# Kernel tuning notes

Measured on AMD Instinct MI355X. Metric: run time of the kernel, lower is better.

The kernel has to match this reference:

```python
import jax, jax.numpy as jnp
import numpy as np

MESH_SIZE = 0.01
HIDDEN = 256
NUM_LAYERS = 3
TEMP = 1e-3          # soft-relay temperature (forward default)
H_SCALE = 0.0        # soft-magnet: mu0*H << B
M_SCALE = 0.5
M_OFFSET = 0.5


def _make_mesh():
    # Uniform triangular Preisach mesh: points (beta, alpha) with 0 <= beta <= alpha <= 1.
    k = int(round(1.0 / MESH_SIZE)) + 1  # 101 grid lines -> 5151 points
    g = np.linspace(0.0, 1.0, k, dtype=np.float32)
    bb, aa = np.meshgrid(g, g, indexing='ij')
    sel = bb <= aa
    return jnp.asarray(np.stack([bb[sel], aa[sel]], axis=-1))  # [N, 2] = (beta, alpha)


def setup_inputs() -> dict:
    key = jax.random.key(0)
    ks = jax.random.split(key, 10)
    mesh = _make_mesh()                       # [N, 2]
    n = mesh.shape[0]
    B, CTXT, T = 8, 128, 2048
    encoder_input = jax.random.uniform(ks[0], (B, CTXT, 2), dtype=jnp.float32)
    decoder_input = jax.random.uniform(ks[1], (B, T, 1), dtype=jnp.float32)
    initial_states = 2.0 * jax.random.uniform(ks[2], (B, n), dtype=jnp.float32) - 1.0  # s in [-1, 1]
    y0 = jax.random.uniform(ks[3], (B,), dtype=jnp.float32)
    # ResNetMLP density network params (input_dim=2, output_dim=1)
    W_in = jax.random.normal(ks[4], (2, HIDDEN), dtype=jnp.float32) * 0.5
    b_in = jnp.zeros((HIDDEN,), dtype=jnp.float32)
    W_blk = jax.random.normal(ks[5], (NUM_LAYERS, HIDDEN, HIDDEN), dtype=jnp.float32) * (1.0 / np.sqrt(HIDDEN))
    b_blk = jnp.zeros((NUM_LAYERS, HIDDEN), dtype=jnp.float32)
    W_out = jax.random.normal(ks[6], (HIDDEN, 1), dtype=jnp.float32) * (1.0 / np.sqrt(HIDDEN))
    b_out = jnp.zeros((1,), dtype=jnp.float32)
    return {'encoder_input': encoder_input, 'decoder_input': decoder_input,
            'initial_states': initial_states, 'y0': y0, 'mesh': mesh,
            'W_in': W_in, 'b_in': b_in, 'W_blk': W_blk, 'b_blk': b_blk,
            'W_out': W_out, 'b_out': b_out}


def _density(mesh, W_in, b_in, W_blk, b_blk, W_out, b_out):
    # ResNetMLP (eval: dropout off) + sigmoid (normalized_density=True)
    h = jax.nn.relu(mesh @ W_in + b_in)
    for i in range(NUM_LAYERS):  # small fixed layer loop
        h = h + jax.nn.relu(h @ W_blk[i] + b_blk[i])
    return jax.nn.sigmoid((h @ W_out + b_out)[..., 0])  # [N]


def _get_states(h_seq, alpha, beta, s0, h0):
    # Sequential soft-relay hysteron update across time.
    # h_seq [B,T], alpha/beta [N], s0 [B,N], h0 [B]
    def step(carry, h_t):  # h_t [B]
        s, h_prev = carry
        up = jax.nn.sigmoid((h_t[:, None] - alpha[None, :]) / TEMP)   # switch to +1 when h > alpha
        dn = jax.nn.sigmoid((h_t[:, None] - beta[None, :]) / TEMP)    # stay/unswitch vs beta when sweeping down
        s_up = s + (1.0 - s) * up            # increasing field branch
        s_dn = -1.0 + (s + 1.0) * dn         # decreasing field branch
        inc = (h_t >= h_prev)[:, None]
        s_new = jnp.where(inc, s_up, s_dn)
        return (s_new, h_t), s_new
    (_, _), states = jax.lax.scan(step, (s0, h0), jnp.swapaxes(h_seq, 0, 1))
    return jnp.swapaxes(states, 0, 1)  # [B, T, N]


def reference(encoder_input, decoder_input, initial_states, y0, mesh,
              W_in, b_in, W_blk, b_blk, W_out, b_out):
    B = encoder_input.shape[0]
    n = mesh.shape[0]
    beta = mesh[:, 0]
    alpha = mesh[:, 1]
    density = _density(mesh, W_in, b_in, W_blk, b_blk, W_out, b_out)  # [N] (shared mesh, eval)
    h = decoder_input[..., 0]                                          # [B, T]
    states = _get_states(h, alpha, beta, initial_states, y0)           # [B, T, N]
    m = jnp.einsum('n,btn->bt', density, states) / jnp.sum(density)    # [B, T]
    b_norm = H_SCALE * h + M_SCALE * m + M_OFFSET
    density_b = jnp.broadcast_to(density, (B, n))
    mesh_b = jnp.broadcast_to(mesh, (B,) + mesh.shape)
    return (b_norm, density_b, m, initial_states, mesh_b)
```

## Files before the change

kernel.cpp:

```cpp
#include <hip/hip_runtime.h>
#include <hip/hip_fp16.h>
#include <math.h>

#define N_MESH   5151
#define NB       8
#define TT       2048
#define HID      256
#define NLAYERS  3
#define NCHUNK   64
#define CHUNK    32
#define NQ       11
#define NPAD     5632
#define SCAN_GRID 512
#define PREP_NBLK 48
#define COPY_NBLK 61
#define MLP_NBLK  81
#define PH2_NBLK  88
#define DENSB_NBLK 21

#define OFF_TP    144
#define SMEM1     656
#define OFF_RED   656
#define OFF_DRED  5264
#define SMEM3     5392

#define WS_DENSITY 0
#define WS_WT      6144
#define WS_PQ      104448

#define OUT_BNORM  0
#define OUT_DENSB  16384
#define OUT_M      57592
#define OUT_S0     73976
#define OUT_MESHB  115184

typedef _Float16 half8  __attribute__((ext_vector_type(8)));
typedef float    f32x4  __attribute__((ext_vector_type(4)));

__device__ __forceinline__ float sigmoid_fast(float x) {
    float e = __expf(-x);
    return __builtin_amdgcn_rcpf(1.0f + e);
}

__device__ __forceinline__ int swz(int row, int kbyte) {
    return row * 512 + (kbyte ^ ((row & 7) << 4));
}

__device__ __forceinline__ float dpp16_sum(float v) {
    int a;
    a = __builtin_amdgcn_update_dpp(0, __float_as_int(v), 0xB1, 0xF, 0xF, true);
    v += __int_as_float(a);
    a = __builtin_amdgcn_update_dpp(0, __float_as_int(v), 0x4E, 0xF, 0xF, true);
    v += __int_as_float(a);
    a = __builtin_amdgcn_update_dpp(0, __float_as_int(v), 0x141, 0xF, 0xF, true);
    v += __int_as_float(a);
    a = __builtin_amdgcn_update_dpp(0, __float_as_int(v), 0x140, 0xF, 0xF, true);
    v += __int_as_float(a);
    return v;
}

__device__ __forceinline__ void build_params(int tid, const float* hs2,
                                             float4* tp)
{
    if (tid < CHUNK) {
        float ht = hs2[tid + 1];
        float hp = hs2[tid];
        bool inc = (ht >= hp);
        float sg = inc ? 1.f : -1.f;
        float psg = sg;
        if (tid > 0) psg = (hs2[tid] >= hs2[tid - 1]) ? 1.f : -1.f;
        float x = ht * 1000.f;
        float gc = rintf(ht * 100.f);
        float4 p;
        p.x = psg - sg;
        if (inc) {
            float Ac = sigmoid_fast(fmaf(10.f, gc, -x));
            p.y = 1.f;  p.z = Ac - gc;
        } else {
            float Ac = sigmoid_fast(fmaf(-10.f, gc, x));
            p.y = -1.f; p.z = gc + Ac;
        }
        p.w = sg;
        tp[tid] = p;
    }
}

__global__ __launch_bounds__(512, 4) void k1_scan1_prep(
    const float* __restrict__ dec, const float* __restrict__ y0,
    const float* __restrict__ mesh, const float* __restrict__ Wblk,
    float2* __restrict__ PQ, half8* __restrict__ WT,
    const float* __restrict__ s0, float* __restrict__ out)
{
    __shared__ __align__(16) char smem[SMEM1];
    const int tid = threadIdx.x;
    const int bid = blockIdx.x;

    if (bid >= SCAN_GRID + PREP_NBLK) {
        int idx = bid - (SCAN_GRID + PREP_NBLK);
        const int n1 = NB * N_MESH;
        const int total = 3 * n1;
#pragma unroll
        for (int k = 0; k < 4; ++k) {
            int j = idx * 2048 + k * 512 + tid;
            if (j < total) {
                if (j < n1) out[OUT_S0 + j] = s0[j];
                else {
                    int jj = j - n1;
                    out[OUT_MESHB + jj] = mesh[jj % (2 * N_MESH)];
                }
            }
        }
        return;
    }

    if (bid >= SCAN_GRID) {
        int g = (bid - SCAN_GRID) * 512 + tid;
        int l  = g & 63;
        int nt = (g >> 6) & 15;
        int kg = (g >> 10) & 7;
        int L  = g >> 13;
        int n  = nt * 16 + (l & 15);
        int kb = kg * 32 + ((l >> 4) & 3) * 8;
        const float* Wb = Wblk + (size_t)L * HID * HID;
        half8 v;
#pragma unroll
        for (int i = 0; i < 8; ++i)
            v[i] = (_Float16)Wb[(size_t)(kb + i) * HID + n];
        WT[g] = v;
        return;
    }

    float* hs2 = (float*)smem;
    float4* tp = (float4*)(smem + OFF_TP);

    const int b = bid & 7;
    const int c = bid >> 3;
    const int t0 = c * CHUNK;

    if (tid < CHUNK) hs2[tid + 1] = dec[b * TT + t0 + tid];
    if (tid == 0) hs2[0] = (c == 0) ? y0[b] : dec[b * TT + t0 - 1];

    float fga[NQ], fgb[NQ];
#pragma unroll
    for (int q = 0; q < NQ; ++q) {
        int n = q * 512 + tid;
        if (n < N_MESH) {
            fgb[q] = rintf(mesh[2 * n]     * 100.0f);
            fga[q] = rintf(mesh[2 * n + 1] * 100.0f);
        } else { fga[q] = 0.f; fgb[q] = 0.f; }
    }
    __syncthreads();
    build_params(tid, hs2, tp);
    __syncthreads();

    float P[NQ], R[NQ];
    float sg0 = tp[0].w;
#pragma unroll
    for (int q = 0; q < NQ; ++q) { P[q] = 1.f; R[q] = -sg0; }

    for (int tb = 0; tb < CHUNK; tb += 8) {
#pragma unroll
        for (int j = 0; j < 8; ++j) {
            float4 p = tp[tb + j];
            bool inc = p.y > 0.f;
#pragma unroll
            for (int q = 0; q < NQ; ++q) {
                float gq = inc ? fga[q] : fgb[q];
                float A = __builtin_amdgcn_fmed3f(fmaf(p.y, gq, p.z), 0.f, 1.f);
                float r = R[q] + p.x;
                P[q] *= A;
                R[q] = r * A;
            }
        }
    }
    float sgl = tp[CHUNK - 1].w;
    size_t basew = ((size_t)(c * NB + b)) * NPAD;
#pragma unroll
    for (int q = 0; q < NQ; ++q) {
        float2 v; v.x = P[q]; v.y = R[q] + sgl;
        PQ[basew + q * 512 + tid] = v;
    }
}

__global__ __launch_bounds__(512) void k2_mlp_phase2(
    const float* __restrict__ mesh, const float* __restrict__ Win,
    const float* __restrict__ bin,  const half8* __restrict__ WT,
    const float* __restrict__ bblk, const float* __restrict__ Wout,
    const float* __restrict__ bout, float* __restrict__ density,
    const float* __restrict__ s0_in, float* __restrict__ PQf)
{
    __shared__ __align__(16) char hA[64 * 512];
    __shared__ float psum[4][16][2];
    const int tid  = threadIdx.x;

    if (blockIdx.x >= MLP_NBLK) {
        int idx = blockIdx.x - MLP_NBLK;
        int nbb = idx % NQ;
        int b   = idx / NQ;
        int n   = nbb * 512 + tid;
        const float2* PQ = (const float2*)PQf;
        float s = (n < N_MESH) ? s0_in[b * N_MESH + n] : 0.f;
#pragma unroll 4
        for (int c = 0; c < NCHUNK; ++c) {
            size_t ix = ((size_t)(c * NB + b)) * NPAD + n;
            float2 pv = PQ[ix];
            PQf[2 * ix] = s;
            s = fmaf(pv.x, s, pv.y);
        }
        return;
    }

    const int w    = tid >> 6;
    const int lane = tid & 63;
    const int rl   = lane & 15;
    const int cg   = lane >> 4;
    const int mt   = w & 3;
    const int nh   = w >> 2;
    const int row0 = blockIdx.x * 64;

    float hreg[8][4];

    {
        float m0[4], m1[4];
#pragma unroll
        for (int r = 0; r < 4; ++r) {
            int gr = row0 + mt * 16 + cg * 4 + r;
            if (gr < N_MESH) { m0[r] = mesh[2 * gr]; m1[r] = mesh[2 * gr + 1]; }
            else { m0[r] = 0.f; m1[r] = 0.f; }
        }
#pragma unroll
        for (int j = 0; j < 8; ++j) {
            int col = nh * 128 + j * 16 + rl;
            float wa = Win[col], wb = Win[HID + col], bi = bin[col];
#pragma unroll
            for (int r = 0; r < 4; ++r) {
                float v = fmaxf(fmaf(m0[r], wa, fmaf(m1[r], wb, bi)), 0.f);
                hreg[j][r] = v;
                *(_Float16*)(hA + swz(mt * 16 + cg * 4 + r, col * 2)) =
                    (_Float16)v;
            }
        }
    }
    __syncthreads();

    for (int L = 0; L < NLAYERS; ++L) {
        half8 af[8];
#pragma unroll
        for (int kg = 0; kg < 8; ++kg)
            af[kg] = *(const half8*)(hA + swz(mt * 16 + rl, kg * 64 + cg * 16));
        __syncthreads();

        float bias[8];
#pragma unroll
        for (int j = 0; j < 8; ++j)
            bias[j] = bblk[L * HID + nh * 128 + j * 16 + rl];

        f32x4 acc[8];
#pragma unroll
        for (int j = 0; j < 8; ++j) acc[j] = (f32x4){0.f, 0.f, 0.f, 0.f};

        const half8* WTL = WT + ((size_t)(L * 8) * 16 + nh * 8) * 64 + lane;
        half8 b0[8], b1[8];
#pragma unroll
        for (int j = 0; j < 8; ++j) b0[j] = WTL[(size_t)j * 64];
#pragma unroll
        for (int kg2 = 0; kg2 < 8; kg2 += 2) {
#pragma unroll
            for (int j = 0; j < 8; ++j)
                b1[j] = WTL[(size_t)(kg2 + 1) * 1024 + (size_t)j * 64];
#pragma unroll
            for (int j = 0; j < 8; ++j)
                acc[j] = __builtin_amdgcn_mfma_f32_16x16x32_f16(
                    af[kg2], b0[j], acc[j], 0, 0, 0);
            if (kg2 + 2 < 8) {
#pragma unroll
                for (int j = 0; j < 8; ++j)
                    b0[j] = WTL[(size_t)(kg2 + 2) * 1024 + (size_t)j * 64];
            }
#pragma unroll
            for (int j = 0; j < 8; ++j)
                acc[j] = __builtin_amdgcn_mfma_f32_16x16x32_f16(
                    af[kg2 + 1], b1[j], acc[j], 0, 0, 0);
        }

#pragma unroll
        for (int j = 0; j < 8; ++j) {
            int col = nh * 128 + j * 16 + rl;
#pragma unroll
            for (int r = 0; r < 4; ++r) {
                float v = hreg[j][r] + fmaxf(acc[j][r] + bias[j], 0.f);
                hreg[j][r] = v;
                if (L < NLAYERS - 1)
                    *(_Float16*)(hA + swz(mt * 16 + cg * 4 + r, col * 2)) =
                        (_Float16)v;
            }
        }
        if (L < NLAYERS - 1) __syncthreads();
    }

    {
        float p[4] = {0.f, 0.f, 0.f, 0.f};
#pragma unroll
        for (int j = 0; j < 8; ++j) {
            float wo = Wout[nh * 128 + j * 16 + rl];
#pragma unroll
            for (int r = 0; r < 4; ++r) p[r] = fmaf(hreg[j][r], wo, p[r]);
        }
#pragma unroll
        for (int st = 1; st < 16; st <<= 1)
#pragma unroll
            for (int r = 0; r < 4; ++r) p[r] += __shfl_xor(p[r], st, 64);
        if (rl == 0) {
#pragma unroll
            for (int r = 0; r < 4; ++r) psum[mt][cg * 4 + r][nh] = p[r];
        }
    }
    __syncthreads();
    if (tid < 64) {
        int gr = row0 + tid;
        float pp = psum[tid >> 4][tid & 15][0] + psum[tid >> 4][tid & 15][1];
        if (gr < N_MESH) density[gr] = sigmoid_fast(pp + bout[0]);
    }
}

__global__ __launch_bounds__(512, 4) void k3_phase3_fin(
    const float* __restrict__ dec, const float* __restrict__ y0,
    const float* __restrict__ mesh, const float* __restrict__ density,
    const float* __restrict__ PQf, float* __restrict__ out)
{
    __shared__ __align__(16) char smem[SMEM3];
    const int tid = threadIdx.x;
    const int bid = blockIdx.x;

    if (bid >= SCAN_GRID) {
        int idx = bid - SCAN_GRID;
#pragma unroll
        for (int k = 0; k < 4; ++k) {
            int j = idx * 2048 + k * 512 + tid;
            if (j < NB * N_MESH) out[OUT_DENSB + j] = density[j % N_MESH];
        }
        return;
    }

    float* hs2 = (float*)smem;
    float4* tp = (float4*)(smem + OFF_TP);
    float* red  = (float*)(smem + OFF_RED);
    float* Dred = (float*)(smem + OFF_DRED);

    const int b = bid & 7;
    const int c = bid >> 3;
    const int t0 = c * CHUNK;

    if (tid < CHUNK) hs2[tid + 1] = dec[b * TT + t0 + tid];
    if (tid == 0) hs2[0] = (c == 0) ? y0[b] : dec[b * TT + t0 - 1];

    float fga[NQ], fgb[NQ];
    float d[NQ], S[NQ];
#pragma unroll
    for (int q = 0; q < NQ; ++q) {
        int n = q * 512 + tid;
        if (n < N_MESH) {
            fgb[q] = rintf(mesh[2 * n]     * 100.0f);
            fga[q] = rintf(mesh[2 * n + 1] * 100.0f);
            d[q]  = density[n];
            S[q]  = PQf[2 * (((size_t)(c * NB + b)) * NPAD + n)];
        } else { fga[q] = 0.f; fgb[q] = 0.f; d[q] = 0.f; S[q] = 0.f; }
    }
    {
        float Dp = 0.f;
#pragma unroll
        for (int q = 0; q < NQ; ++q) Dp += d[q];
        Dp = dpp16_sum(Dp);
        if ((tid & 15) == 0) Dred[tid >> 4] = Dp;
    }
    __syncthreads();
    build_params(tid, hs2, tp);
    __syncthreads();

    float z[NQ];
    float sg0 = tp[0].w;
#pragma unroll
    for (int q = 0; q < NQ; ++q) z[q] = S[q] - sg0;

    for (int tb = 0; tb < CHUNK; tb += 8) {
        float v[8];
#pragma unroll
        for (int j = 0; j < 8; ++j) {
            float4 p = tp[tb + j];
            bool inc = p.y > 0.f;
            float a0 = 0.f, a1 = 0.f;
#pragma unroll
            for (int q = 0; q < NQ; ++q) {
                float gq = inc ? fga[q] : fgb[q];
                float A = __builtin_amdgcn_fmed3f(fmaf(p.y, gq, p.z), 0.f, 1.f);
                float zn = (z[q] + p.x) * A;
                z[q] = zn;
                if (q & 1) a1 = fmaf(d[q], zn, a1);
                else       a0 = fmaf(d[q], zn, a0);
            }
            v[j] = a0 + a1;
        }
#pragma unroll
        for (int j = 0; j < 8; ++j) v[j] = dpp16_sum(v[j]);
        float outv = v[0];
#pragma unroll
        for (int j = 1; j < 8; ++j) if ((tid & 15) == j) outv = v[j];
        if ((tid & 15) < 8)
            red[(tb + (tid & 15)) * 36 + (tid >> 4)] = outv;
    }
    __syncthreads();

    if (tid < CHUNK) {
        float acc = 0.f;
#pragma unroll
        for (int g4 = 0; g4 < 32; g4 += 4) {
            float4 r4 = *(const float4*)&red[tid * 36 + g4];
            acc += (r4.x + r4.y) + (r4.z + r4.w);
        }
        float D = 0.f;
#pragma unroll
        for (int g4 = 0; g4 < 32; g4 += 4) {
            float4 d4 = *(const float4*)&Dred[g4];
            D += (d4.x + d4.y) + (d4.z + d4.w);
        }
        float gd = tp[tid].w;
        int t = t0 + tid;
        float m = (acc + gd * D) / D;
        out[OUT_M + b * TT + t] = m;
        out[OUT_BNORM + b * TT + t] = 0.5f * m + 0.5f;
    }
}

extern "C" void kernel_launch(void* const* d_in, const int* in_sizes, int n_in,
                              void* d_out, int out_size, void* d_ws, size_t ws_size,
                              hipStream_t stream) {
    const float* dec  = (const float*)d_in[1];
    const float* s0   = (const float*)d_in[2];
    const float* y0   = (const float*)d_in[3];
    const float* mesh = (const float*)d_in[4];
    const float* Win  = (const float*)d_in[5];
    const float* bin  = (const float*)d_in[6];
    const float* Wblk = (const float*)d_in[7];
    const float* bblk = (const float*)d_in[8];
    const float* Wout = (const float*)d_in[9];
    const float* bout = (const float*)d_in[10];
    float* out = (float*)d_out;
    float* ws  = (float*)d_ws;

    float*  density  = ws + WS_DENSITY;
    half8*  wt       = (half8*)(ws + WS_WT);
    float*  pqf      = ws + WS_PQ;
    float2* pq       = (float2*)pqf;

    k1_scan1_prep<<<SCAN_GRID + PREP_NBLK + COPY_NBLK, 512, 0, stream>>>(
        dec, y0, mesh, Wblk, pq, wt, s0, out);
    k2_mlp_phase2<<<MLP_NBLK + PH2_NBLK, 512, 0, stream>>>(
        mesh, Win, bin, wt, bblk, Wout, bout, density, s0, pqf);
    k3_phase3_fin<<<SCAN_GRID + DENSB_NBLK, 512, 0, stream>>>(
        dec, y0, mesh, density, pqf, out);
}
```

Baseline: 67.07 us.

## Specialize relay scan loops by direction and zero-delta, store carry states densely

The inner relay-update loops in both scan kernels are split into four uniform branches on field direction and on whether the per-step delta is zero. This removes the per-element select and multiply by p.y, and skips the add when the delta is zero. Phase-2 carry states now go to a separate dense workspace array instead of being strided into the PQ float2 buffer, so phase-3 reads are contiguous, and mesh loads are vectorized as float2. The branches rely on p.y being ±1 (the fmaf with p.y becomes a plain add or subtract) and they increase code size.

```diff
diff --git a/kernel.cpp b/kernel.cpp
--- a/kernel.cpp
+++ b/kernel.cpp
@@ -27,6 +27,7 @@
 #define WS_DENSITY 0
 #define WS_WT      6144
 #define WS_PQ      104448
+#define WS_S       5871616
 
 #define OUT_BNORM  0
 #define OUT_DENSB  16384
@@ -145,8 +146,9 @@
     for (int q = 0; q < NQ; ++q) {
         int n = q * 512 + tid;
         if (n < N_MESH) {
-            fgb[q] = rintf(mesh[2 * n]     * 100.0f);
-            fga[q] = rintf(mesh[2 * n + 1] * 100.0f);
+            float2 mv = *(const float2*)&mesh[2 * n];
+            fgb[q] = rintf(mv.x * 100.0f);
+            fga[q] = rintf(mv.y * 100.0f);
         } else { fga[q] = 0.f; fgb[q] = 0.f; }
     }
     __syncthreads();
@@ -163,13 +165,39 @@
         for (int j = 0; j < 8; ++j) {
             float4 p = tp[tb + j];
             bool inc = p.y > 0.f;
-#pragma unroll
-            for (int q = 0; q < NQ; ++q) {
-                float gq = inc ? fga[q] : fgb[q];
-                float A = __builtin_amdgcn_fmed3f(fmaf(p.y, gq, p.z), 0.f, 1.f);
-                float r = R[q] + p.x;
-                P[q] *= A;
-                R[q] = r * A;
+            bool dl0 = p.x == 0.f;
+            if (inc) {
+                if (dl0) {
+#pragma unroll
+                    for (int q = 0; q < NQ; ++q) {
+                        float A = __builtin_amdgcn_fmed3f(fga[q] + p.z, 0.f, 1.f);
+                        P[q] *= A;
+                        R[q] *= A;
+                    }
+                } else {
+#pragma unroll
+                    for (int q = 0; q < NQ; ++q) {
+                        float A = __builtin_amdgcn_fmed3f(fga[q] + p.z, 0.f, 1.f);
+                        P[q] *= A;
+                        R[q] = (R[q] + p.x) * A;
+                    }
+                }
+            } else {
+                if (dl0) {
+#pragma unroll
+                    for (int q = 0; q < NQ; ++q) {
+                        float A = __builtin_amdgcn_fmed3f(p.z - fgb[q], 0.f, 1.f);
+                        P[q] *= A;
+                        R[q] *= A;
+                    }
+                } else {
+#pragma unroll
+                    for (int q = 0; q < NQ; ++q) {
+                        float A = __builtin_amdgcn_fmed3f(p.z - fgb[q], 0.f, 1.f);
+                        P[q] *= A;
+                        R[q] = (R[q] + p.x) * A;
+                    }
+                }
             }
         }
     }
@@ -187,7 +215,8 @@
     const float* __restrict__ bin,  const half8* __restrict__ WT,
     const float* __restrict__ bblk, const float* __restrict__ Wout,
     const float* __restrict__ bout, float* __restrict__ density,
-    const float* __restrict__ s0_in, float* __restrict__ PQf)
+    const float* __restrict__ s0_in, const float2* __restrict__ PQ,
+    float* __restrict__ Sarr)
 {
     __shared__ __align__(16) char hA[64 * 512];
     __shared__ float psum[4][16][2];
@@ -198,13 +227,12 @@
         int nbb = idx % NQ;
         int b   = idx / NQ;
         int n   = nbb * 512 + tid;
-        const float2* PQ = (const float2*)PQf;
         float s = (n < N_MESH) ? s0_in[b * N_MESH + n] : 0.f;
 #pragma unroll 4
         for (int c = 0; c < NCHUNK; ++c) {
             size_t ix = ((size_t)(c * NB + b)) * NPAD + n;
             float2 pv = PQ[ix];
-            PQf[2 * ix] = s;
+            Sarr[ix] = s;
             s = fmaf(pv.x, s, pv.y);
         }
         return;
@@ -326,7 +354,7 @@
 __global__ __launch_bounds__(512, 4) void k3_phase3_fin(
     const float* __restrict__ dec, const float* __restrict__ y0,
     const float* __restrict__ mesh, const float* __restrict__ density,
-    const float* __restrict__ PQf, float* __restrict__ out)
+    const float* __restrict__ Sarr, float* __restrict__ out)
 {
     __shared__ __align__(16) char smem[SMEM3];
     const int tid = threadIdx.x;
@@ -360,10 +388,11 @@
     for (int q = 0; q < NQ; ++q) {
         int n = q * 512 + tid;
         if (n < N_MESH) {
-            fgb[q] = rintf(mesh[2 * n]     * 100.0f);
-            fga[q] = rintf(mesh[2 * n + 1] * 100.0f);
+            float2 mv = *(const float2*)&mesh[2 * n];
+            fgb[q] = rintf(mv.x * 100.0f);
+            fga[q] = rintf(mv.y * 100.0f);
             d[q]  = density[n];
-            S[q]  = PQf[2 * (((size_t)(c * NB + b)) * NPAD + n)];
+            S[q]  = Sarr[((size_t)(c * NB + b)) * NPAD + n];
         } else { fga[q] = 0.f; fgb[q] = 0.f; d[q] = 0.f; S[q] = 0.f; }
     }
     {
@@ -388,15 +417,48 @@
         for (int j = 0; j < 8; ++j) {
             float4 p = tp[tb + j];
             bool inc = p.y > 0.f;
+            bool dl0 = p.x == 0.f;
             float a0 = 0.f, a1 = 0.f;
-#pragma unroll
-            for (int q = 0; q < NQ; ++q) {
-                float gq = inc ? fga[q] : fgb[q];
-                float A = __builtin_amdgcn_fmed3f(fmaf(p.y, gq, p.z), 0.f, 1.f);
-                float zn = (z[q] + p.x) * A;
-                z[q] = zn;
-                if (q & 1) a1 = fmaf(d[q], zn, a1);
-                else       a0 = fmaf(d[q], zn, a0);
+            if (inc) {
+                if (dl0) {
+#pragma unroll
+                    for (int q = 0; q < NQ; ++q) {
+                        float A = __builtin_amdgcn_fmed3f(fga[q] + p.z, 0.f, 1.f);
+                        float zn = z[q] * A;
+                        z[q] = zn;
+                        if (q & 1) a1 = fmaf(d[q], zn, a1);
+                        else       a0 = fmaf(d[q], zn, a0);
+                    }
+                } else {
+#pragma unroll
+                    for (int q = 0; q < NQ; ++q) {
+                        float A = __builtin_amdgcn_fmed3f(fga[q] + p.z, 0.f, 1.f);
+                        float zn = (z[q] + p.x) * A;
+                        z[q] = zn;
+                        if (q & 1) a1 = fmaf(d[q], zn, a1);
+                        else       a0 = fmaf(d[q], zn, a0);
+                    }
+                }
+            } else {
+                if (dl0) {
+#pragma unroll
+                    for (int q = 0; q < NQ; ++q) {
+                        float A = __builtin_amdgcn_fmed3f(p.z - fgb[q], 0.f, 1.f);
+                        float zn = z[q] * A;
+                        z[q] = zn;
+                        if (q & 1) a1 = fmaf(d[q], zn, a1);
+                        else       a0 = fmaf(d[q], zn, a0);
+                    }
+                } else {
+#pragma unroll
+                    for (int q = 0; q < NQ; ++q) {
+                        float A = __builtin_amdgcn_fmed3f(p.z - fgb[q], 0.f, 1.f);
+                        float zn = (z[q] + p.x) * A;
+                        z[q] = zn;
+                        if (q & 1) a1 = fmaf(d[q], zn, a1);
+                        else       a0 = fmaf(d[q], zn, a0);
+                    }
+                }
             }
             v[j] = a0 + a1;
         }
@@ -451,11 +513,12 @@
     half8*  wt       = (half8*)(ws + WS_WT);
     float*  pqf      = ws + WS_PQ;
     float2* pq       = (float2*)pqf;
+    float*  sarr     = ws + WS_S;
 
     k1_scan1_prep<<<SCAN_GRID + PREP_NBLK + COPY_NBLK, 512, 0, stream>>>(
         dec, y0, mesh, Wblk, pq, wt, s0, out);
     k2_mlp_phase2<<<MLP_NBLK + PH2_NBLK, 512, 0, stream>>>(
-        mesh, Win, bin, wt, bblk, Wout, bout, density, s0, pqf);
+        mesh, Win, bin, wt, bblk, Wout, bout, density, s0, pq, sarr);
     k3_phase3_fin<<<SCAN_GRID + DENSB_NBLK, 512, 0, stream>>>(
-        dec, y0, mesh, density, pqf, out);
-}
+        dec, y0, mesh, density, sarr, out);
+}
```

Result: faster. 61.07 us, median of 3 (-8.9%).
